# Performance work log

Hardware: AMD Instinct MI355X
Metric: run time of the kernel (lower is better)

Reference implementation:

```python
import jax, jax.numpy as jnp
import numpy as np

WH, WW = 7, 7
N = WH * WW
H = 16          # num_heads
D = 32          # head_dim
NW = 64         # num windows per image (mask.shape[0])


def _relative_position_index(wh, ww):
    coords = np.stack(np.meshgrid(np.arange(wh), np.arange(ww), indexing='ij'))  # (2, wh, ww)
    cf = coords.reshape(2, -1)                                                   # (2, N)
    rel = cf[:, :, None] - cf[:, None, :]                                        # (2, N, N)
    rel = rel.transpose(1, 2, 0).copy()
    rel[:, :, 0] += wh - 1
    rel[:, :, 1] += ww - 1
    rel[:, :, 0] *= 2 * ww - 1
    return rel.sum(-1)  # (N, N) int

REL_IDX = jnp.asarray(_relative_position_index(WH, WW))


def setup_inputs() -> dict:
    key = jax.random.key(0)
    ks = jax.random.split(key, 5)
    B_ = 2048
    dim = H * D
    x = jax.random.normal(ks[0], (B_, N, dim), dtype=jnp.float32)
    mask = jnp.zeros((NW, N, N), dtype=jnp.float32)
    rpb_table = jax.random.normal(ks[1], ((2 * WH - 1) * (2 * WW - 1), H), dtype=jnp.float32) * 0.02
    qkv_w = jax.random.normal(ks[2], (3 * dim, dim), dtype=jnp.float32) * (dim ** -0.5)
    qkv_b = jnp.zeros((3 * dim,), dtype=jnp.float32)
    proj_w = jax.random.normal(ks[3], (dim, dim), dtype=jnp.float32) * (dim ** -0.5)
    proj_b = jnp.zeros((dim,), dtype=jnp.float32)
    return {"x": x, "mask": mask, "rpb_table": rpb_table,
            "qkv_w": qkv_w, "qkv_b": qkv_b, "proj_w": proj_w, "proj_b": proj_b}


def reference(x, mask, rpb_table, qkv_w, qkv_b, proj_w, proj_b):
    B_, n, C = x.shape
    scale = D ** -0.5
    # qkv projection (torch Linear: x @ W^T + b)
    qkv = (x @ qkv_w.T + qkv_b).reshape(B_, n, 3, H, D)
    q = qkv[:, :, 0].transpose(0, 2, 1, 3) * scale  # (B_, H, N, D)
    k = qkv[:, :, 1].transpose(0, 2, 1, 3)
    v = qkv[:, :, 2].transpose(0, 2, 1, 3)
    attn = jnp.einsum('bhnd,bhmd->bhnm', q, k)      # (B_, H, N, N)
    # relative position bias: gather (N*N,) rows from table -> (N, N, H) -> (H, N, N)
    bias = rpb_table[REL_IDX.reshape(-1)].reshape(n, n, H).transpose(2, 0, 1)
    attn = attn + bias[None]
    # shifted-window mask add: (B, nW, H, N, N) + (1, nW, 1, N, N)
    nW = mask.shape[0]
    attn = attn.reshape(B_ // nW, nW, H, n, n) + mask[None, :, None]
    attn = attn.reshape(B_, H, n, n)
    attn = jax.nn.softmax(attn, axis=-1)
    out = jnp.einsum('bhnm,bhmd->bhnd', attn, v)    # (B_, H, N, D)
    out = out.transpose(0, 2, 1, 3).reshape(B_, n, H * D)
    return out @ proj_w.T + proj_b
```

## Files before the change

kernel.cpp:

```cpp
#include <hip/hip_runtime.h>

typedef _Float16 f16;
typedef _Float16 f16x8 __attribute__((ext_vector_type(8)));
typedef _Float16 f16x4 __attribute__((ext_vector_type(4)));
typedef __fp16 fp16x2 __attribute__((ext_vector_type(2)));
typedef float f32x4 __attribute__((ext_vector_type(4)));

#define NTOK 49
#define NH 16
#define HD 32
#define DIM 512
#define NWIN 64
#define NB 2048
#define MTOT (NB*NTOK)
#define SCALE 0.17677669529663687f
#define VTS 56

__device__ __forceinline__ void gload_lds16(const f16* g, f16* l) {
    __builtin_amdgcn_global_load_lds((const __attribute__((address_space(1))) void*)g,
                                     (__attribute__((address_space(3))) void*)l, 16, 0, 0);
}

__device__ __forceinline__ void cvt_body(const float* __restrict__ s, f16* __restrict__ d,
                                         int n4, int bid, int nb) {
    int i = bid * 256 + threadIdx.x;
    int st = nb * 256;
    for (; i < n4; i += st) {
        float4 v = ((const float4*)s)[i];
        f16x4 o = { (f16)v.x, (f16)v.y, (f16)v.z, (f16)v.w };
        *(f16x4*)(d + (size_t)i * 4) = o;
    }
}

__global__ __launch_bounds__(256) void prep_kernel(const float* __restrict__ rpb,
                                                   const float* __restrict__ mask,
                                                   f16* __restrict__ comb2,
                                                   const float* __restrict__ qkvw,
                                                   f16* __restrict__ w16,
                                                   const float* __restrict__ projw,
                                                   f16* __restrict__ pw16,
                                                   const float* __restrict__ x,
                                                   f16* __restrict__ x16) {
    const int bid = blockIdx.x;
    if (bid >= 16384) {
        if (bid < 16384 + 2048)      cvt_body(x, x16, MTOT * DIM / 4, bid - 16384, 2048);
        else if (bid < 16384 + 2816) cvt_body(qkvw, w16, 1536 * 512 / 4, bid - 16384 - 2048, 768);
        else                         cvt_body(projw, pw16, 512 * 512 / 4, bid - 16384 - 2816, 256);
        return;
    }
    int idx = bid * 256 + threadIdx.x;
    int r4   = idx & 3;
    int tj   = (idx >> 2) & 3;
    int ti   = (idx >> 4) & 3;
    int lane = (idx >> 6) & 63;
    int wh   = idx >> 12;
    int h = wh & 15, w = wh >> 4;
    int g = lane >> 4, c16 = lane & 15;
    int k = ti * 16 + g * 4 + r4;
    int q = tj * 16 + c16;
    float v;
    if (k >= NTOK)      v = -30000.f;
    else if (q >= NTOK) v = 0.f;
    else {
        int rq = q / 7, cq = q - rq * 7;
        int rk = k / 7, ck = k - rk * 7;
        int rel = (rq - rk + 6) * 13 + (cq - ck + 6);
        v = rpb[rel * NH + h] + mask[(w * NTOK + q) * NTOK + k];
    }
    comb2[idx] = (f16)v;
}

#define WAIT_LGKM  asm volatile("s_waitcnt lgkmcnt(0)" ::: "memory")
#define WAIT_VM(N) asm volatile("s_waitcnt vmcnt(" #N ")" ::: "memory")

template<int NT>
__global__ __launch_bounds__(512) void gemm256(const f16* __restrict__ A,
                                               const f16* __restrict__ Bw,
                                               const float* __restrict__ bias,
                                               f16* __restrict__ qo,
                                               f16* __restrict__ ko,
                                               f16* __restrict__ vto) {
    __shared__ __align__(16) f16 As[2][256][64];
    __shared__ __align__(16) f16 Bs[2][256][64];

    const int tid = threadIdx.x;
    const int lane = tid & 63;
    const int wv = tid >> 6;
    const int wm = wv >> 2, wn = wv & 3;
    const int g = lane >> 4, c16 = lane & 15;

    const int nblk = gridDim.x;
    const int f = blockIdx.x;
    const int work = (f & 7) * (nblk >> 3) + (f >> 3);
    const int m0 = (work / NT) * 256;
    const int n0 = (work % NT) * 256;

    const int srow = lane >> 3;
    const int schunk = (lane & 7) ^ srow;
    const f16* gA = A  + (size_t)(m0 + wv * 16 + srow) * DIM + schunk * 8;
    const f16* gB = Bw + (size_t)(n0 + wv * 16 + srow) * DIM + schunk * 8;

#define STAGE1(buf, kt, role) do {                                             \
    const f16* _s = (((role) < 2) ? gA : gB) + (size_t)(((role) & 1) * 128) * DIM + (kt) * 64; \
    f16* _d = ((role) < 2) ? &As[buf][((role) & 1) * 128 + wv * 16][0]         \
                           : &Bs[buf][((role) & 1) * 128 + wv * 16][0];        \
    gload_lds16(_s, _d);                                                       \
    gload_lds16(_s + (size_t)8 * DIM, _d + 8 * 64);                            \
} while (0)
#define STAGE_T(buf, kt) do { STAGE1(buf, kt, 0); STAGE1(buf, kt, 1);          \
                              STAGE1(buf, kt, 2); STAGE1(buf, kt, 3); } while (0)

#define READS(buf, kk, AF, BF) do {                                            \
    _Pragma("unroll") for (int _i = 0; _i < 8; ++_i)                           \
        (AF)[_i] = *(const f16x8*)&As[buf][wm * 128 + _i * 16 + c16][(((kk) * 4 + g) ^ (c16 & 7)) * 8]; \
    _Pragma("unroll") for (int _j = 0; _j < 4; ++_j)                           \
        (BF)[_j] = *(const f16x8*)&Bs[buf][wn * 64 + _j * 16 + c16][(((kk) * 4 + g) ^ (c16 & 7)) * 8]; \
} while (0)

#define MM(AF, BF) do {                                                        \
    __builtin_amdgcn_s_setprio(1);                                             \
    _Pragma("unroll") for (int _j = 0; _j < 4; ++_j)                           \
    _Pragma("unroll") for (int _i = 0; _i < 8; ++_i)                           \
        acc[_j][_i] = __builtin_amdgcn_mfma_f32_16x16x32_f16((BF)[_j], (AF)[_i], acc[_j][_i], 0, 0, 0); \
    __builtin_amdgcn_s_setprio(0);                                             \
} while (0)

    f32x4 acc[4][8];
#pragma unroll
    for (int j = 0; j < 4; ++j)
#pragma unroll
        for (int i = 0; i < 8; ++i)
            acc[j][i] = (f32x4){0.f, 0.f, 0.f, 0.f};

    f16x8 a0[8], b0[4], a1[8], b1[4];

    const int KT = DIM / 64;

    STAGE_T(0, 0);
    STAGE_T(1, 1);
    WAIT_VM(8);
    __builtin_amdgcn_s_barrier();
    READS(0, 0, a0, b0);

#pragma unroll
    for (int t = 0; t < KT; ++t) {
        const int b = t & 1, nb = b ^ 1;

        READS(b, 1, a1, b1);
        MM(a0, b0);
        WAIT_LGKM;
        __builtin_amdgcn_s_barrier();
        if (t + 2 < KT) STAGE_T(b, t + 2);
        if (t + 2 < KT) { WAIT_VM(8); }
        else if (t + 1 < KT) { WAIT_VM(0); }

        if (t + 1 < KT) READS(nb, 0, a0, b0);
        MM(a1, b1);
    }
#undef STAGE1
#undef STAGE_T
#undef READS
#undef MM

#pragma unroll
    for (int i = 0; i < 8; ++i) {
        const int m = m0 + wm * 128 + i * 16 + c16;
        const int bb = m / NTOK, tk = m - (m / NTOK) * NTOK;
#pragma unroll
        for (int j = 0; j < 4; ++j) {
            const int n = n0 + wn * 64 + j * 16 + g * 4;
            f32x4 v = acc[j][i];
            const f32x4 b4 = *(const f32x4*)&bias[n];
            v += b4;
            const int s = n >> 9;
            const int hh = (n >> 5) & 15;
            const int d0 = n & 31;
            const size_t bh = (size_t)(bb * NH + hh);
            if (s == 0) {
                f16x4 o = { (f16)(v[0] * SCALE), (f16)(v[1] * SCALE),
                            (f16)(v[2] * SCALE), (f16)(v[3] * SCALE) };
                *(f16x4*)(qo + (bh * NTOK + tk) * HD + d0) = o;
            } else if (s == 1) {
                f16x4 o = { (f16)v[0], (f16)v[1], (f16)v[2], (f16)v[3] };
                *(f16x4*)(ko + (bh * NTOK + tk) * HD + d0) = o;
            } else {
#pragma unroll
                for (int r = 0; r < 4; ++r)
                    vto[(bh * HD + d0 + r) * VTS + tk] = (f16)v[r];
            }
        }
    }
}

__global__ __launch_bounds__(256, 3) void gemm128(const f16* __restrict__ A,
                                                  const f16* __restrict__ Bw,
                                                  const float* __restrict__ bias,
                                                  float* __restrict__ outp) {
    __shared__ __align__(16) f16 As[3][128][32];
    __shared__ __align__(16) f16 Bs[3][128][32];

    const int NT = 4;
    const int tid = threadIdx.x;
    const int lane = tid & 63;
    const int wv = tid >> 6;
    const int wr = wv >> 1, wc = wv & 1;
    const int g = lane >> 4, c16 = lane & 15;
    const int rsw = (c16 >> 1) & 3;

    const int nblk = gridDim.x;
    const int f = blockIdx.x;
    const int work = (f & 7) * (nblk >> 3) + (f >> 3);
    const int m0 = (work / NT) * 128;
    const int n0 = (work % NT) * 128;

    const int srow = lane >> 2;
    const int schunk = (lane & 3) ^ ((srow >> 1) & 3);
    const f16* gA = A  + (size_t)(m0 + wv * 32 + srow) * DIM + schunk * 8;
    const f16* gB = Bw + (size_t)(n0 + wv * 32 + srow) * DIM + schunk * 8;

#define STAGE6(buf, t) do { \
    gload_lds16(gA + (t) * 32,                     &As[buf][wv * 32][0]);      \
    gload_lds16(gA + (size_t)16 * DIM + (t) * 32,  &As[buf][wv * 32 + 16][0]); \
    gload_lds16(gB + (t) * 32,                     &Bs[buf][wv * 32][0]);      \
    gload_lds16(gB + (size_t)16 * DIM + (t) * 32,  &Bs[buf][wv * 32 + 16][0]); \
} while (0)

    f32x4 acc[4][4];
#pragma unroll
    for (int j = 0; j < 4; ++j)
#pragma unroll
        for (int i = 0; i < 4; ++i)
            acc[j][i] = (f32x4){0.f, 0.f, 0.f, 0.f};

    STAGE6(0, 0);
    STAGE6(1, 1);
    WAIT_VM(4);
    __builtin_amdgcn_s_barrier();

    const int KS = DIM / 32;
#pragma unroll
    for (int t = 0; t < KS; ++t) {
        const int cb = t % 3;
        if (t + 2 < KS) STAGE6((t + 2) % 3, t + 2);
        f16x8 af[4], bf[4];
#pragma unroll
        for (int i = 0; i < 4; ++i)
            af[i] = *(const f16x8*)&As[cb][wr * 64 + i * 16 + c16][(g ^ rsw) * 8];
#pragma unroll
        for (int j = 0; j < 4; ++j)
            bf[j] = *(const f16x8*)&Bs[cb][wc * 64 + j * 16 + c16][(g ^ rsw) * 8];
        __builtin_amdgcn_s_setprio(1);
#pragma unroll
        for (int j = 0; j < 4; ++j)
#pragma unroll
            for (int i = 0; i < 4; ++i)
                acc[j][i] = __builtin_amdgcn_mfma_f32_16x16x32_f16(bf[j], af[i], acc[j][i], 0, 0, 0);
        __builtin_amdgcn_s_setprio(0);
        WAIT_LGKM;
        __builtin_amdgcn_sched_barrier(0);
        if (t + 2 < KS) {
            WAIT_VM(4);
        } else if (t + 1 < KS) {
            WAIT_VM(0);
        }
        if (t + 1 < KS) __builtin_amdgcn_s_barrier();
    }
#undef STAGE6

#pragma unroll
    for (int i = 0; i < 4; ++i) {
        const int m = m0 + wr * 64 + i * 16 + c16;
#pragma unroll
        for (int j = 0; j < 4; ++j) {
            const int n = n0 + wc * 64 + j * 16 + g * 4;
            f32x4 v = acc[j][i];
            const f32x4 b4 = *(const f32x4*)&bias[n];
            v += b4;
            float4 o = { v[0], v[1], v[2], v[3] };
            *(float4*)(outp + (size_t)m * DIM + n) = o;
        }
    }
}

__global__ __launch_bounds__(256) void attn_kernel(const f16* __restrict__ qw,
                                                   const f16* __restrict__ kw,
                                                   const f16* __restrict__ vt,
                                                   const f16* __restrict__ comb2,
                                                   f16* __restrict__ aout) {
    __shared__ __align__(16) f16 Ps[4][64][72];

    const int wv = threadIdx.x >> 6;
    const int l = threadIdx.x & 63;
    const int f = blockIdx.x;
    const int work = (f & 7) * (gridDim.x >> 3) + (f >> 3);
    const int bid = work * 4 + wv;
    const int b = bid >> 4, h = bid & 15;
    const int w = b & (NWIN - 1);
    const int g = l >> 4, c16 = l & 15;
    const size_t qkbase = (size_t)bid * (NTOK * HD);
    const size_t vbase = (size_t)bid * (HD * VTS);

    const f16x8 z8 = {};

    f16x8 qf[4], kf[4];
#pragma unroll
    for (int t = 0; t < 4; ++t) {
        int row = t * 16 + c16;
        f16x8 q = z8, k = z8;
        if (row < NTOK) {
            q = *(const f16x8*)(qw + qkbase + row * HD + g * 8);
            k = *(const f16x8*)(kw + qkbase + row * HD + g * 8);
        }
        qf[t] = q; kf[t] = k;
    }

    const f16* cb = comb2 + (((size_t)(w * NH + h) * 64 + l) << 6);
    f16x8 cbv[8];
#pragma unroll
    for (int k = 0; k < 8; ++k) cbv[k] = *(const f16x8*)(cb + k * 8);
    f32x4 St[4][4];
#pragma unroll
    for (int i = 0; i < 4; ++i)
#pragma unroll
        for (int j = 0; j < 4; ++j) {
            const int e = i * 16 + j * 4;
#pragma unroll
            for (int r = 0; r < 4; ++r)
                St[i][j][r] = (float)cbv[(e + r) >> 3][(e + r) & 7];
        }
#pragma unroll
    for (int i = 0; i < 4; ++i)
#pragma unroll
        for (int j = 0; j < 4; ++j)
            St[i][j] = __builtin_amdgcn_mfma_f32_16x16x32_f16(kf[i], qf[j], St[i][j], 0, 0, 0);

    float inv[4];
#pragma unroll
    for (int j = 0; j < 4; ++j) {
        float m = St[0][j][0];
#pragma unroll
        for (int i = 0; i < 4; ++i)
#pragma unroll
            for (int r = 0; r < 4; ++r) m = fmaxf(m, St[i][j][r]);
        m = fmaxf(m, __shfl_xor(m, 16, 64));
        m = fmaxf(m, __shfl_xor(m, 32, 64));
        float s = 0.f;
#pragma unroll
        for (int i = 0; i < 4; ++i)
#pragma unroll
            for (int r = 0; r < 4; ++r) {
                float p = __expf(St[i][j][r] - m);
                St[i][j][r] = p;
                s += p;
            }
        s += __shfl_xor(s, 16, 64);
        s += __shfl_xor(s, 32, 64);
        inv[j] = 1.f / s;
    }

#pragma unroll
    for (int j = 0; j < 4; ++j) {
        const int q = j * 16 + c16;
#pragma unroll
        for (int i = 0; i < 4; ++i) {
            fp16x2 u0 = __builtin_amdgcn_cvt_pkrtz(St[i][j][0], St[i][j][1]);
            fp16x2 u1 = __builtin_amdgcn_cvt_pkrtz(St[i][j][2], St[i][j][3]);
            *(fp16x2*)&Ps[wv][q][i * 16 + 4 * g]     = u0;
            *(fp16x2*)&Ps[wv][q][i * 16 + 4 * g + 2] = u1;
        }
    }
    WAIT_LGKM;

    f32x4 O2[2][4];
    const f32x4 zf = (f32x4){0.f, 0.f, 0.f, 0.f};
#pragma unroll
    for (int td = 0; td < 2; ++td)
#pragma unroll
        for (int ti = 0; ti < 4; ++ti) O2[td][ti] = zf;
#pragma unroll
    for (int c = 0; c < 2; ++c) {
        f16x8 pf[4], vf[2];
#pragma unroll
        for (int ti = 0; ti < 4; ++ti)
            pf[ti] = *(const f16x8*)&Ps[wv][ti * 16 + c16][c * 32 + g * 8];
        int tcol = c * 32 + g * 8;
#pragma unroll
        for (int td = 0; td < 2; ++td) {
            f16x8 vv = z8;
            if (tcol < VTS)
                vv = *(const f16x8*)(vt + vbase + (size_t)(td * 16 + c16) * VTS + tcol);
            vf[td] = vv;
        }
#pragma unroll
        for (int td = 0; td < 2; ++td)
#pragma unroll
            for (int ti = 0; ti < 4; ++ti)
                O2[td][ti] = __builtin_amdgcn_mfma_f32_16x16x32_f16(vf[td], pf[ti], O2[td][ti], 0, 0, 0);
    }

#pragma unroll
    for (int ti = 0; ti < 4; ++ti) {
        int tok = ti * 16 + c16;
        if (tok < NTOK) {
            size_t ob = ((size_t)(b * NTOK + tok)) * DIM + h * HD;
#pragma unroll
            for (int td = 0; td < 2; ++td) {
                f32x4 v = O2[td][ti];
                float iv = inv[ti];
                f16x4 o = { (f16)(v[0] * iv), (f16)(v[1] * iv),
                            (f16)(v[2] * iv), (f16)(v[3] * iv) };
                *(f16x4*)(aout + ob + td * 16 + g * 4) = o;
            }
        }
    }
}

extern "C" void kernel_launch(void* const* d_in, const int* in_sizes, int n_in,
                              void* d_out, int out_size, void* d_ws, size_t ws_size,
                              hipStream_t stream) {
    const float* x      = (const float*)d_in[0];
    const float* mask   = (const float*)d_in[1];
    const float* rpb    = (const float*)d_in[2];
    const float* qkv_w  = (const float*)d_in[3];
    const float* qkv_b  = (const float*)d_in[4];
    const float* proj_w = (const float*)d_in[5];
    const float* proj_b = (const float*)d_in[6];
    float* out = (float*)d_out;

    char* ws = (char*)d_ws;
    size_t o = 0;
    f16* x16   = (f16*)(ws + o); o += (size_t)MTOT * DIM * 2;
    f16* w16   = (f16*)(ws + o); o += (size_t)1536 * 512 * 2;
    f16* pw16  = (f16*)(ws + o); o += (size_t)512 * 512 * 2;
    f16* qws   = (f16*)(ws + o); o += (size_t)NB * NH * NTOK * HD * 2;
    f16* kws   = (f16*)(ws + o); o += (size_t)NB * NH * NTOK * HD * 2;
    f16* vtws  = (f16*)(ws + o); o += (size_t)NB * NH * HD * VTS * 2;
    f16* cb2   = (f16*)(ws + o);
    f16* aout = x16;

    prep_kernel<<<dim3(16384 + 2048 + 768 + 256), dim3(256), 0, stream>>>(
        rpb, mask, cb2, qkv_w, w16, proj_w, pw16, x, x16);

    gemm256<6><<<dim3((MTOT / 256) * 6), dim3(512), 0, stream>>>(
        x16, w16, qkv_b, qws, kws, vtws);

    attn_kernel<<<dim3(NB * NH / 4), dim3(256), 0, stream>>>(qws, kws, vtws, cb2, aout);

    gemm128<<<dim3((MTOT / 128) * 4), dim3(256), 0, stream>>>(
        aout, pw16, proj_b, out);
}
```

Before: 529.7 us.

## Shrink QKV GEMM tile to 128x256 with BK=32 for higher occupancy

```diff
diff --git a/kernel.cpp b/kernel.cpp
--- a/kernel.cpp
+++ b/kernel.cpp
@@ -74,97 +74,79 @@
 #define WAIT_VM(N) asm volatile("s_waitcnt vmcnt(" #N ")" ::: "memory")
 
 template<int NT>
-__global__ __launch_bounds__(512) void gemm256(const f16* __restrict__ A,
-                                               const f16* __restrict__ Bw,
-                                               const float* __restrict__ bias,
-                                               f16* __restrict__ qo,
-                                               f16* __restrict__ ko,
-                                               f16* __restrict__ vto) {
-    __shared__ __align__(16) f16 As[2][256][64];
-    __shared__ __align__(16) f16 Bs[2][256][64];
+__global__ __launch_bounds__(512, 4) void gemm_qkv(const f16* __restrict__ A,
+                                                   const f16* __restrict__ Bw,
+                                                   const float* __restrict__ bias,
+                                                   f16* __restrict__ qo,
+                                                   f16* __restrict__ ko,
+                                                   f16* __restrict__ vto) {
+    __shared__ __align__(16) f16 As[2][128][32];
+    __shared__ __align__(16) f16 Bs[2][256][32];
 
     const int tid = threadIdx.x;
     const int lane = tid & 63;
     const int wv = tid >> 6;
     const int wm = wv >> 2, wn = wv & 3;
     const int g = lane >> 4, c16 = lane & 15;
+    const int rsw = (c16 >> 1) & 3;
 
     const int nblk = gridDim.x;
     const int f = blockIdx.x;
     const int work = (f & 7) * (nblk >> 3) + (f >> 3);
-    const int m0 = (work / NT) * 256;
+    const int m0 = (work / NT) * 128;
     const int n0 = (work % NT) * 256;
 
-    const int srow = lane >> 3;
-    const int schunk = (lane & 7) ^ srow;
+    const int srow = lane >> 2;
+    const int schunk = (lane & 3) ^ ((srow >> 1) & 3);
     const f16* gA = A  + (size_t)(m0 + wv * 16 + srow) * DIM + schunk * 8;
-    const f16* gB = Bw + (size_t)(n0 + wv * 16 + srow) * DIM + schunk * 8;
-
-#define STAGE1(buf, kt, role) do {                                             \
-    const f16* _s = (((role) < 2) ? gA : gB) + (size_t)(((role) & 1) * 128) * DIM + (kt) * 64; \
-    f16* _d = ((role) < 2) ? &As[buf][((role) & 1) * 128 + wv * 16][0]         \
-                           : &Bs[buf][((role) & 1) * 128 + wv * 16][0];        \
-    gload_lds16(_s, _d);                                                       \
-    gload_lds16(_s + (size_t)8 * DIM, _d + 8 * 64);                            \
+    const f16* gB = Bw + (size_t)(n0 + wv * 32 + srow) * DIM + schunk * 8;
+
+#define STAGE(buf, t) do { const int _k = (t) * 32;                            \
+    gload_lds16(gA + _k,                       &As[buf][wv * 16][0]);          \
+    gload_lds16(gB + _k,                       &Bs[buf][wv * 32][0]);          \
+    gload_lds16(gB + (size_t)16 * DIM + _k,    &Bs[buf][wv * 32 + 16][0]);     \
 } while (0)
-#define STAGE_T(buf, kt) do { STAGE1(buf, kt, 0); STAGE1(buf, kt, 1);          \
-                              STAGE1(buf, kt, 2); STAGE1(buf, kt, 3); } while (0)
-
-#define READS(buf, kk, AF, BF) do {                                            \
-    _Pragma("unroll") for (int _i = 0; _i < 8; ++_i)                           \
-        (AF)[_i] = *(const f16x8*)&As[buf][wm * 128 + _i * 16 + c16][(((kk) * 4 + g) ^ (c16 & 7)) * 8]; \
-    _Pragma("unroll") for (int _j = 0; _j < 4; ++_j)                           \
-        (BF)[_j] = *(const f16x8*)&Bs[buf][wn * 64 + _j * 16 + c16][(((kk) * 4 + g) ^ (c16 & 7)) * 8]; \
-} while (0)
-
-#define MM(AF, BF) do {                                                        \
-    __builtin_amdgcn_s_setprio(1);                                             \
-    _Pragma("unroll") for (int _j = 0; _j < 4; ++_j)                           \
-    _Pragma("unroll") for (int _i = 0; _i < 8; ++_i)                           \
-        acc[_j][_i] = __builtin_amdgcn_mfma_f32_16x16x32_f16((BF)[_j], (AF)[_i], acc[_j][_i], 0, 0, 0); \
-    __builtin_amdgcn_s_setprio(0);                                             \
-} while (0)
-
-    f32x4 acc[4][8];
+
+    f32x4 acc[4][4];
 #pragma unroll
     for (int j = 0; j < 4; ++j)
 #pragma unroll
-        for (int i = 0; i < 8; ++i)
+        for (int i = 0; i < 4; ++i)
             acc[j][i] = (f32x4){0.f, 0.f, 0.f, 0.f};
 
-    f16x8 a0[8], b0[4], a1[8], b1[4];
-
-    const int KT = DIM / 64;
-
-    STAGE_T(0, 0);
-    STAGE_T(1, 1);
-    WAIT_VM(8);
+    STAGE(0, 0);
+    WAIT_VM(0);
     __builtin_amdgcn_s_barrier();
-    READS(0, 0, a0, b0);
-
-#pragma unroll
-    for (int t = 0; t < KT; ++t) {
+
+    const int KS = DIM / 32;
+#pragma unroll
+    for (int t = 0; t < KS; ++t) {
         const int b = t & 1, nb = b ^ 1;
-
-        READS(b, 1, a1, b1);
-        MM(a0, b0);
+        if (t + 1 < KS) STAGE(nb, t + 1);
+        f16x8 af[4], bf[4];
+#pragma unroll
+        for (int i = 0; i < 4; ++i)
+            af[i] = *(const f16x8*)&As[b][wm * 64 + i * 16 + c16][(g ^ rsw) * 8];
+#pragma unroll
+        for (int j = 0; j < 4; ++j)
+            bf[j] = *(const f16x8*)&Bs[b][wn * 64 + j * 16 + c16][(g ^ rsw) * 8];
+        __builtin_amdgcn_s_setprio(1);
+#pragma unroll
+        for (int j = 0; j < 4; ++j)
+#pragma unroll
+            for (int i = 0; i < 4; ++i)
+                acc[j][i] = __builtin_amdgcn_mfma_f32_16x16x32_f16(bf[j], af[i], acc[j][i], 0, 0, 0);
+        __builtin_amdgcn_s_setprio(0);
         WAIT_LGKM;
+        __builtin_amdgcn_sched_barrier(0);
+        if (t + 1 < KS) WAIT_VM(0);
         __builtin_amdgcn_s_barrier();
-        if (t + 2 < KT) STAGE_T(b, t + 2);
-        if (t + 2 < KT) { WAIT_VM(8); }
-        else if (t + 1 < KT) { WAIT_VM(0); }
-
-        if (t + 1 < KT) READS(nb, 0, a0, b0);
-        MM(a1, b1);
-    }
-#undef STAGE1
-#undef STAGE_T
-#undef READS
-#undef MM
-
-#pragma unroll
-    for (int i = 0; i < 8; ++i) {
-        const int m = m0 + wm * 128 + i * 16 + c16;
+    }
+#undef STAGE
+
+#pragma unroll
+    for (int i = 0; i < 4; ++i) {
+        const int m = m0 + wm * 64 + i * 16 + c16;
         const int bb = m / NTOK, tk = m - (m / NTOK) * NTOK;
 #pragma unroll
         for (int j = 0; j < 4; ++j) {
@@ -441,7 +423,7 @@
     prep_kernel<<<dim3(16384 + 2048 + 768 + 256), dim3(256), 0, stream>>>(
         rpb, mask, cb2, qkv_w, w16, proj_w, pw16, x, x16);
 
-    gemm256<6><<<dim3((MTOT / 256) * 6), dim3(512), 0, stream>>>(
+    gemm_qkv<6><<<dim3((MTOT / 128) * 6), dim3(512), 0, stream>>>(
         x16, w16, qkv_b, qws, kws, vtws);
 
     attn_kernel<<<dim3(NB * NH / 4), dim3(256), 0, stream>>>(qws, kws, vtws, cb2, aout);
```

Measured after the change: 570.1 us. 1.08x slower.
